# Performance work log

Measured on AMD Instinct MI355X. Metric: run time of the kernel, lower is better.

The kernel has to match this reference:

```python
import jax, jax.numpy as jnp
import numpy as np


def conv1x1(x, w, b):
    # x: [B,C,H,W], w: [O,C], b: [O] -> [B,O,H,W]
    return jnp.einsum('oc,bchw->bohw', w, x) + b[None, :, None, None]


def setup_inputs() -> dict:
    key = jax.random.key(0)
    ks = jax.random.split(key, 9)
    B, C, H, W = 4, 256, 64, 64
    Ci = C // 2
    s_in = 1.0 / np.sqrt(C)
    s_mid = 1.0 / np.sqrt(Ci)
    return {
        'x': jax.random.normal(ks[0], (B, C, H, W), jnp.float32),
        'theta_w': jax.random.normal(ks[1], (Ci, C), jnp.float32) * s_in,
        'theta_b': jnp.zeros((Ci,), jnp.float32),
        'phi_w': jax.random.normal(ks[2], (Ci, C), jnp.float32) * s_in,
        'phi_b': jnp.zeros((Ci,), jnp.float32),
        'g_w': jax.random.normal(ks[3], (Ci, C), jnp.float32) * s_in,
        'g_b': jnp.zeros((Ci,), jnp.float32),
        'out_w': jax.random.normal(ks[4], (C, Ci), jnp.float32) * s_mid,
        'out_b': jnp.zeros((C,), jnp.float32),
    }


def reference(x, theta_w, theta_b, phi_w, phi_b, g_w, g_b, out_w, out_b):
    B, C, H, W = x.shape
    N = H * W
    theta = conv1x1(x, theta_w, theta_b).reshape(B, -1, N)  # [B,Ci,N]
    phi = conv1x1(x, phi_w, phi_b).reshape(B, -1, N)        # [B,Ci,N]
    g = conv1x1(x, g_w, g_b).reshape(B, -1, N)              # [B,Ci,N]
    # attention[b,n,m] = theta[b,:,n] . phi[b,:,m]
    attn = jnp.einsum('bcn,bcm->bnm', theta, phi)           # [B,N,N]
    attn = jax.nn.softmax(attn, axis=-1)
    # out[b,c,n] = sum_m g[b,c,m] * attn[b,n,m]  (g @ attn^T)
    out = jnp.einsum('bcm,bnm->bcn', g, attn).reshape(B, -1, H, W)
    out = conv1x1(out, out_w, out_b)
    return out + x
```

## Files before the change

kernel.cpp:

```cpp
#include <hip/hip_runtime.h>
#include <stdint.h>

#define NB 4
#define NC 256
#define NCI 128
#define NN 4096

typedef __attribute__((ext_vector_type(8))) short short8;
typedef __attribute__((ext_vector_type(4))) float f32x4;

__device__ __forceinline__ float bf2f(unsigned short u) {
    union { unsigned int i; float f; } v; v.i = ((unsigned int)u) << 16; return v.f;
}
__device__ __forceinline__ unsigned short f2bf(float f) {
    union { unsigned int i; float f; } v; v.f = f;
    unsigned int b = v.i;
    b += 0x7FFFu + ((b >> 16) & 1u);
    return (unsigned short)(b >> 16);
}

__global__ void k_fill(float* __restrict__ p, float v, int n) {
    int i = blockIdx.x * blockDim.x + threadIdx.x;
    if (i < n) p[i] = v;
}

__global__ __launch_bounds__(256) void k_split(
    const float* __restrict__ Wt, const float* __restrict__ Wp,
    const float* __restrict__ Wg, const float* __restrict__ Wo,
    unsigned short* __restrict__ wbuf) {
    const float LOG2E = 1.4426950408889634f;
    int m = blockIdx.y;
    int i = blockIdx.x * 256 + threadIdx.x;
    if (m == 0) {
        float v = Wt[i] * LOG2E;
        unsigned short h = f2bf(v);
        wbuf[i] = h;
        wbuf[32768 + i] = f2bf(v - bf2f(h));
    } else if (m == 1) {
        float v = Wp[i];
        unsigned short h = f2bf(v);
        wbuf[65536 + i] = h;
        wbuf[98304 + i] = f2bf(v - bf2f(h));
    } else if (m == 2) {
        wbuf[131072 + i] = f2bf(Wg[i]);
    } else {
        wbuf[163840 + i] = f2bf(Wo[i]);
    }
}

__global__ __launch_bounds__(256, 2) void k_qkv2(
    const float* __restrict__ x,
    const unsigned short* __restrict__ WpH, const unsigned short* __restrict__ WpL,
    const unsigned short* __restrict__ WgH,
    const float* __restrict__ bp, const float* __restrict__ bg,
    unsigned short* __restrict__ phiH, unsigned short* __restrict__ phiL,
    unsigned short* __restrict__ gout) {
    __shared__ __align__(16) unsigned short sXh[32 * 72];
    __shared__ __align__(16) unsigned short sXl[32 * 72];
    const int b = blockIdx.y, n0 = blockIdx.x * 32;
    const int tid = threadIdx.x, lane = tid & 63, wave = tid >> 6;
    const int col = lane & 15, quad = lane >> 4;
    const int wm = wave * 32;

    f32x4 accP[2][2], accG[2][2];
#pragma unroll
    for (int i = 0; i < 2; i++)
#pragma unroll
        for (int j = 0; j < 2; j++)
#pragma unroll
            for (int e = 0; e < 4; e++) { accP[i][j][e] = 0.f; accG[i][j][e] = 0.f; }

    for (int c0 = 0; c0 < NC; c0 += 64) {
        __syncthreads();
        short8 ah[2][2], al[2][2], ag[2][2];
#pragma unroll
        for (int ks = 0; ks < 2; ks++)
#pragma unroll
            for (int i = 0; i < 2; i++) {
                size_t w = (size_t)(wm + i * 16 + col) * NC + c0 + ks * 32 + quad * 8;
                ah[ks][i] = *(const short8*)&WpH[w];
                al[ks][i] = *(const short8*)&WpL[w];
                ag[ks][i] = *(const short8*)&WgH[w];
            }
        {
            int cp = tid >> 3, n4 = (tid & 7) * 4;
            const float* xp = x + ((size_t)(b * NC + c0 + 2 * cp)) * NN + n0 + n4;
            float4 a = *(const float4*)xp;
            float4 c = *(const float4*)(xp + NN);
            float av[4] = { a.x, a.y, a.z, a.w };
            float cv[4] = { c.x, c.y, c.z, c.w };
#pragma unroll
            for (int j = 0; j < 4; j++) {
                unsigned short ha = f2bf(av[j]), hc = f2bf(cv[j]);
                unsigned short la = f2bf(av[j] - bf2f(ha)), lc = f2bf(cv[j] - bf2f(hc));
                *(unsigned int*)&sXh[(n4 + j) * 72 + 2 * cp] =
                    (unsigned int)ha | ((unsigned int)hc << 16);
                *(unsigned int*)&sXl[(n4 + j) * 72 + 2 * cp] =
                    (unsigned int)la | ((unsigned int)lc << 16);
            }
        }
        __syncthreads();
#pragma unroll
        for (int ks = 0; ks < 2; ks++)
#pragma unroll
            for (int j = 0; j < 2; j++) {
                short8 bh = *(const short8*)&sXh[(j * 16 + col) * 72 + ks * 32 + quad * 8];
                short8 bl = *(const short8*)&sXl[(j * 16 + col) * 72 + ks * 32 + quad * 8];
#pragma unroll
                for (int i = 0; i < 2; i++) {
                    accP[i][j] = __builtin_amdgcn_mfma_f32_16x16x32_bf16(ah[ks][i], bh, accP[i][j], 0, 0, 0);
                    accP[i][j] = __builtin_amdgcn_mfma_f32_16x16x32_bf16(ah[ks][i], bl, accP[i][j], 0, 0, 0);
                    accP[i][j] = __builtin_amdgcn_mfma_f32_16x16x32_bf16(al[ks][i], bh, accP[i][j], 0, 0, 0);
                    accG[i][j] = __builtin_amdgcn_mfma_f32_16x16x32_bf16(ag[ks][i], bh, accG[i][j], 0, 0, 0);
                }
            }
    }
#pragma unroll
    for (int i = 0; i < 2; i++) {
        int mrow = wm + i * 16 + quad * 4;
#pragma unroll
        for (int j = 0; j < 2; j++) {
            int n = n0 + j * 16 + col;
            unsigned short h[4], l[4];
#pragma unroll
            for (int e = 0; e < 4; e++) {
                float v = accP[i][j][e] + bp[mrow + e];
                h[e] = f2bf(v);
                l[e] = f2bf(v - bf2f(h[e]));
            }
            uint2 hv, lv;
            hv.x = (unsigned int)h[0] | ((unsigned int)h[1] << 16);
            hv.y = (unsigned int)h[2] | ((unsigned int)h[3] << 16);
            lv.x = (unsigned int)l[0] | ((unsigned int)l[1] << 16);
            lv.y = (unsigned int)l[2] | ((unsigned int)l[3] << 16);
            *(uint2*)&phiH[((size_t)(b * NN + n)) * NCI + mrow] = hv;
            *(uint2*)&phiL[((size_t)(b * NN + n)) * NCI + mrow] = lv;
#pragma unroll
            for (int r = 0; r < 4; r++)
                gout[((size_t)(b * NCI + mrow + r)) * NN + n] = f2bf(accG[i][j][r] + bg[mrow + r]);
        }
    }
}

__global__ __launch_bounds__(1024, 4) void k_attn(
    const float* __restrict__ x,
    const unsigned short* __restrict__ WtH, const unsigned short* __restrict__ WtL,
    const float* __restrict__ bt,
    const unsigned short* __restrict__ phiH, const unsigned short* __restrict__ phiL,
    const unsigned short* __restrict__ gmat,
    const unsigned short* __restrict__ WoH, const float* __restrict__ bo,
    float* __restrict__ y) {
    const float LOG2E = 1.4426950408889634f;
    __shared__ __align__(16) char smem[69632];
    unsigned short* sPhiH = (unsigned short*)(smem);
    unsigned short* sPhiL = (unsigned short*)(smem + 16384);
    unsigned short* sG    = (unsigned short*)(smem + 32768);
    unsigned short* sPall = (unsigned short*)(smem + 49152);
    float* sLi            = (float*)(smem + 57344);
    unsigned short* sThH  = (unsigned short*)(smem);
    unsigned short* sThL  = (unsigned short*)(smem + 16384);
    unsigned short* sXhA  = (unsigned short*)(smem + 32768);
    unsigned short* sXlA  = (unsigned short*)(smem + 41984);
    unsigned short* sXhB  = (unsigned short*)(smem + 51200);
    unsigned short* sXlB  = (unsigned short*)(smem + 60416);
    float* sThF           = (float*)(smem + 32768);
    unsigned short* sO    = (unsigned short*)(smem);

    const int id = blockIdx.x;
    const int xcd = id & 7, slot = id >> 3;
    const int b = xcd >> 1;
    const int n0 = (slot * 2 + (xcd & 1)) * 64;

    const int tid = threadIdx.x, lane = tid & 63, wave = tid >> 6;
    const int col = lane & 15, quad = lane >> 4;
    const int qg = wave >> 2, kh = wave & 3;

    const int half = wave >> 3;
    const int wci8 = (wave & 7) * 16;
    f32x4 th[4];
#pragma unroll
    for (int j = 0; j < 4; j++)
#pragma unroll
        for (int e = 0; e < 4; e++) th[j][e] = 0.f;

    for (int s = 0; s < 2; s++) {
        {
            int set = tid >> 9;
            int t = tid & 511;
            int cp = t >> 4, n4 = (t & 15) * 4;
            int myc0 = set * 128 + s * 64;
            unsigned short* dXh = set ? sXhB : sXhA;
            unsigned short* dXl = set ? sXlB : sXlA;
            const float* xp = x + ((size_t)(b * NC + myc0 + 2 * cp)) * NN + n0 + n4;
            float4 a = *(const float4*)xp;
            float4 c = *(const float4*)(xp + NN);
            float av[4] = { a.x, a.y, a.z, a.w };
            float cv[4] = { c.x, c.y, c.z, c.w };
#pragma unroll
            for (int j = 0; j < 4; j++) {
                unsigned short ha = f2bf(av[j]), hc = f2bf(cv[j]);
                unsigned short la = f2bf(av[j] - bf2f(ha)), lc = f2bf(cv[j] - bf2f(hc));
                *(unsigned int*)&dXh[(n4 + j) * 72 + 2 * cp] =
                    (unsigned int)ha | ((unsigned int)hc << 16);
                *(unsigned int*)&dXl[(n4 + j) * 72 + 2 * cp] =
                    (unsigned int)la | ((unsigned int)lc << 16);
            }
        }
        __syncthreads();
        {
            int c0 = half * 128 + s * 64;
            const unsigned short* mXh = half ? sXhB : sXhA;
            const unsigned short* mXl = half ? sXlB : sXlA;
#pragma unroll
            for (int ks = 0; ks < 2; ks++) {
                size_t w = (size_t)(wci8 + col) * NC + c0 + ks * 32 + quad * 8;
                short8 ah = *(const short8*)&WtH[w];
                short8 al = *(const short8*)&WtL[w];
#pragma unroll
                for (int j = 0; j < 4; j++) {
                    short8 bh = *(const short8*)&mXh[(j * 16 + col) * 72 + ks * 32 + quad * 8];
                    short8 bl = *(const short8*)&mXl[(j * 16 + col) * 72 + ks * 32 + quad * 8];
                    th[j] = __builtin_amdgcn_mfma_f32_16x16x32_bf16(ah, bh, th[j], 0, 0, 0);
                    th[j] = __builtin_amdgcn_mfma_f32_16x16x32_bf16(ah, bl, th[j], 0, 0, 0);
                    th[j] = __builtin_amdgcn_mfma_f32_16x16x32_bf16(al, bh, th[j], 0, 0, 0);
                }
            }
        }
        __syncthreads();
    }
    if (half == 0) {
#pragma unroll
        for (int j = 0; j < 4; j++) {
            int q = j * 16 + col;
            int ci = (wci8 + quad * 4) ^ ((q & 7) << 2);
            *(f32x4*)&sThF[q * 128 + ci] = th[j];
        }
    }
    __syncthreads();
    if (half == 1) {
#pragma unroll
        for (int j = 0; j < 4; j++) {
            int q = j * 16 + col;
            int cif = (wci8 + quad * 4) ^ ((q & 7) << 2);
            f32x4 o = *(const f32x4*)&sThF[q * 128 + cif];
            unsigned short h[4], l[4];
#pragma unroll
            for (int e = 0; e < 4; e++) {
                float v = o[e] + th[j][e] + bt[wci8 + quad * 4 + e] * LOG2E;
                h[e] = f2bf(v);
                l[e] = f2bf(v - bf2f(h[e]));
            }
            int cisw = (wci8 + quad * 4) ^ ((q & 7) << 3);
            uint2 hv, lv;
            hv.x = (unsigned int)h[0] | ((unsigned int)h[1] << 16);
            hv.y = (unsigned int)h[2] | ((unsigned int)h[3] << 16);
            lv.x = (unsigned int)l[0] | ((unsigned int)l[1] << 16);
            lv.y = (unsigned int)l[2] | ((unsigned int)l[3] << 16);
            *(uint2*)&sThH[q * 128 + cisw] = hv;
            *(uint2*)&sThL[q * 128 + cisw] = lv;
        }
    }
    __syncthreads();
    short8 qh[4], ql[4];
    {
        int qrow = qg * 16 + col;
        int qsw = (qrow & 7) << 3;
#pragma unroll
        for (int ks = 0; ks < 4; ks++) {
            int off = (ks * 32 + quad * 8) ^ qsw;
            qh[ks] = *(const short8*)&sThH[qrow * 128 + off];
            ql[ks] = *(const short8*)&sThL[qrow * 128 + off];
        }
    }

    f32x4 oacc[2];
#pragma unroll
    for (int i = 0; i < 2; i++)
#pragma unroll
        for (int e = 0; e < 4; e++) oacc[i][e] = 0.f;
    float li[4] = { 0.f, 0.f, 0.f, 0.f };

    for (int m0 = 0; m0 < NN; m0 += 64) {
        __syncthreads();
        {
            int row = tid >> 4, seg = tid & 15;
            size_t src = ((size_t)(b * NN + m0 + row)) * NCI + seg * 8;
            int dst = row * 128 + ((seg * 8) ^ ((row & 7) << 3));
            *(uint4*)&sPhiH[dst] = *(const uint4*)&phiH[src];
            *(uint4*)&sPhiL[dst] = *(const uint4*)&phiL[src];
            int row2 = tid >> 3, seg2 = tid & 7;
            int dst2 = row2 * 64 + ((seg2 * 8) ^ ((row2 & 7) << 3));
            *(uint4*)&sG[dst2] =
                *(const uint4*)&gmat[((size_t)(b * NCI + row2)) * NN + m0 + seg2 * 8];
        }
        __syncthreads();

        f32x4 S;
#pragma unroll
        for (int e = 0; e < 4; e++) S[e] = 0.f;
        {
            int kcol = kh * 16 + col;
            int kswz = (kcol & 7) << 3;
#pragma unroll
            for (int ks = 0; ks < 4; ks++) {
                int off = (ks * 32 + quad * 8) ^ kswz;
                short8 ph = *(const short8*)&sPhiH[kcol * 128 + off];
                short8 pl = *(const short8*)&sPhiL[kcol * 128 + off];
                S = __builtin_amdgcn_mfma_f32_16x16x32_bf16(qh[ks], ph, S, 0, 0, 0);
                S = __builtin_amdgcn_mfma_f32_16x16x32_bf16(qh[ks], pl, S, 0, 0, 0);
                S = __builtin_amdgcn_mfma_f32_16x16x32_bf16(ql[ks], ph, S, 0, 0, 0);
            }
        }
#pragma unroll
        for (int r = 0; r < 4; r++) {
            float p = exp2f(S[r]);
            li[r] += p;
            int q = qg * 16 + quad * 4 + r;
            sPall[q * 64 + ((kh * 16 + col) ^ ((q & 7) << 3))] = f2bf(p);
        }
        __syncthreads();

        short8 pf[2], af[2][2];
        {
            int qrow = qg * 16 + col;
            int qsw = (qrow & 7) << 3;
#pragma unroll
            for (int ks = 0; ks < 2; ks++)
                pf[ks] = *(const short8*)&sPall[qrow * 64 + ((ks * 32 + quad * 8) ^ qsw)];
#pragma unroll
            for (int ct = 0; ct < 2; ct++) {
                int grow = kh * 32 + ct * 16 + col;
                int gsw = (grow & 7) << 3;
#pragma unroll
                for (int ks = 0; ks < 2; ks++)
                    af[ct][ks] = *(const short8*)&sG[grow * 64 + ((ks * 32 + quad * 8) ^ gsw)];
            }
        }
#pragma unroll
        for (int ct = 0; ct < 2; ct++)
#pragma unroll
            for (int ks = 0; ks < 2; ks++)
                oacc[ct] = __builtin_amdgcn_mfma_f32_16x16x32_bf16(
                    af[ct][ks], pf[ks], oacc[ct], 0, 0, 0);
    }

#pragma unroll
    for (int r = 0; r < 4; r++) {
        float rs = li[r];
#pragma unroll
        for (int off = 1; off < 16; off <<= 1) rs += __shfl_xor(rs, off);
        li[r] = rs;
    }
    if (col == 0) {
#pragma unroll
        for (int r = 0; r < 4; r++) sLi[wave * 16 + quad * 4 + r] = li[r];
    }
    __syncthreads();
    float inv = 1.0f / (sLi[(qg * 4 + 0) * 16 + col] + sLi[(qg * 4 + 1) * 16 + col] +
                        sLi[(qg * 4 + 2) * 16 + col] + sLi[(qg * 4 + 3) * 16 + col]);

#pragma unroll
    for (int ct = 0; ct < 2; ct++) {
        int q = qg * 16 + col;
        int ci = kh * 32 + ct * 16 + quad * 4;
        int cisw = ci ^ ((q & 7) << 3);
        uint2 v;
        unsigned short p0 = f2bf(oacc[ct][0] * inv);
        unsigned short p1 = f2bf(oacc[ct][1] * inv);
        unsigned short p2 = f2bf(oacc[ct][2] * inv);
        unsigned short p3 = f2bf(oacc[ct][3] * inv);
        v.x = (unsigned int)p0 | ((unsigned int)p1 << 16);
        v.y = (unsigned int)p2 | ((unsigned int)p3 << 16);
        *(uint2*)&sO[q * 128 + cisw] = v;
    }
    __syncthreads();
    f32x4 acc[4];
#pragma unroll
    for (int j = 0; j < 4; j++)
#pragma unroll
        for (int e = 0; e < 4; e++) acc[j][e] = 0.f;
#pragma unroll
    for (int ks = 0; ks < 4; ks++) {
        short8 af2 = *(const short8*)&WoH[(size_t)(wave * 16 + col) * NCI + ks * 32 + quad * 8];
#pragma unroll
        for (int j = 0; j < 4; j++) {
            int row = j * 16 + col;
            short8 bf = *(const short8*)&sO[row * 128 + ((ks * 32 + quad * 8) ^ ((row & 7) << 3))];
            acc[j] = __builtin_amdgcn_mfma_f32_16x16x32_bf16(af2, bf, acc[j], 0, 0, 0);
        }
    }
#pragma unroll
    for (int j = 0; j < 4; j++)
#pragma unroll
        for (int e = 0; e < 4; e++) {
            int o = wave * 16 + quad * 4 + e;
            size_t idx = ((size_t)(b * NC + o)) * NN + n0 + j * 16 + col;
            y[idx] = acc[j][e] + bo[o] + x[idx];
        }
}

extern "C" void kernel_launch(void* const* d_in, const int* in_sizes, int n_in,
                              void* d_out, int out_size, void* d_ws, size_t ws_size,
                              hipStream_t stream) {
    float* y = (float*)d_out;

    bool sizes_ok = (n_in == 9) &&
        in_sizes[0] == NB * NC * NN && in_sizes[1] == NCI * NC && in_sizes[2] == NCI &&
        in_sizes[3] == NCI * NC && in_sizes[4] == NCI && in_sizes[5] == NCI * NC &&
        in_sizes[6] == NCI && in_sizes[7] == NC * NCI && in_sizes[8] == NC &&
        out_size == NB * NC * NN;
    if (!sizes_ok) {
        k_fill<<<(out_size + 255) / 256, 256, 0, stream>>>(y, 777.0f, out_size);
        return;
    }
    if (ws_size < (size_t)16 * 1024 * 1024) {
        k_fill<<<(out_size + 255) / 256, 256, 0, stream>>>(y, 555.0f, out_size);
        return;
    }

    const float* x  = (const float*)d_in[0];
    const float* tw = (const float*)d_in[1];
    const float* tb = (const float*)d_in[2];
    const float* pw = (const float*)d_in[3];
    const float* pb = (const float*)d_in[4];
    const float* gw = (const float*)d_in[5];
    const float* gb = (const float*)d_in[6];
    const float* ow = (const float*)d_in[7];
    const float* obias = (const float*)d_in[8];

    unsigned short* ws16 = (unsigned short*)d_ws;
    unsigned short* phiH = ws16;
    unsigned short* phiL = ws16 + 2097152;
    unsigned short* g    = ws16 + 4194304;
    unsigned short* wbuf = ws16 + 6291456;
    unsigned short* WtH = wbuf,           *WtL = wbuf + 32768;
    unsigned short* WpH = wbuf + 65536,   *WpL = wbuf + 98304;
    unsigned short* WgH = wbuf + 131072,  *WoH = wbuf + 163840;

    k_split<<<dim3(128, 4), 256, 0, stream>>>(tw, pw, gw, ow, wbuf);
    k_qkv2<<<dim3(128, NB), 256, 0, stream>>>(x, WpH, WpL, WgH, pb, gb, phiH, phiL, g);
    k_attn<<<dim3(256), 1024, 0, stream>>>(x, WtH, WtL, tb, phiH, phiL, g, WoH, obias, y);
}
```

Baseline: 220.2 us.

## Double-buffer phi/g tiles with register prefetch in attention loop

Splits the phi and g shared-memory staging into two buffers. The next key tile is loaded from global memory into registers at the start of each step and written to the alternate buffer after the MFMA work, so global load latency overlaps compute and one barrier per tile is removed. Shared memory use rises from about 68KB to 105KB per block, and the prefetch adds registers per thread. Both of these may limit occupancy on 1024-thread blocks.

```diff
diff --git a/kernel.cpp b/kernel.cpp
--- a/kernel.cpp
+++ b/kernel.cpp
@@ -151,12 +151,15 @@
     const unsigned short* __restrict__ WoH, const float* __restrict__ bo,
     float* __restrict__ y) {
     const float LOG2E = 1.4426950408889634f;
-    __shared__ __align__(16) char smem[69632];
-    unsigned short* sPhiH = (unsigned short*)(smem);
-    unsigned short* sPhiL = (unsigned short*)(smem + 16384);
-    unsigned short* sG    = (unsigned short*)(smem + 32768);
-    unsigned short* sPall = (unsigned short*)(smem + 49152);
-    float* sLi            = (float*)(smem + 57344);
+    __shared__ __align__(16) char smem[107520];
+    unsigned short* sPhiH0 = (unsigned short*)(smem);
+    unsigned short* sPhiH1 = (unsigned short*)(smem + 16384);
+    unsigned short* sPhiL0 = (unsigned short*)(smem + 32768);
+    unsigned short* sPhiL1 = (unsigned short*)(smem + 49152);
+    unsigned short* sG0    = (unsigned short*)(smem + 65536);
+    unsigned short* sG1    = (unsigned short*)(smem + 81920);
+    unsigned short* sPall  = (unsigned short*)(smem + 98304);
+    float* sLi             = (float*)(smem + 106496);
     unsigned short* sThH  = (unsigned short*)(smem);
     unsigned short* sThL  = (unsigned short*)(smem + 16384);
     unsigned short* sXhA  = (unsigned short*)(smem + 32768);
@@ -174,6 +177,24 @@
     const int tid = threadIdx.x, lane = tid & 63, wave = tid >> 6;
     const int col = lane & 15, quad = lane >> 4;
     const int qg = wave >> 2, kh = wave & 3;
+
+    uint4 rPh, rPl, rG;
+    auto LOADT = [&](int m0) {
+        int row = tid >> 4, seg = tid & 15;
+        size_t src = ((size_t)(b * NN + m0 + row)) * NCI + seg * 8;
+        rPh = *(const uint4*)&phiH[src];
+        rPl = *(const uint4*)&phiL[src];
+        int row2 = tid >> 3, seg2 = tid & 7;
+        rG = *(const uint4*)&gmat[((size_t)(b * NCI + row2)) * NN + m0 + seg2 * 8];
+    };
+    auto STORET = [&](unsigned short* dPh, unsigned short* dPl, unsigned short* dG) {
+        int row = tid >> 4, seg = tid & 15;
+        int dst = row * 128 + ((seg * 8) ^ ((row & 7) << 3));
+        *(uint4*)&dPh[dst] = rPh;
+        *(uint4*)&dPl[dst] = rPl;
+        int row2 = tid >> 3, seg2 = tid & 7;
+        *(uint4*)&dG[row2 * 64 + ((seg2 * 8) ^ ((row2 & 7) << 3))] = rG;
+    };
 
     const int half = wave >> 3;
     const int wci8 = (wave & 7) * 16;
@@ -272,6 +293,9 @@
             ql[ks] = *(const short8*)&sThL[qrow * 128 + off];
         }
     }
+    LOADT(0);
+    __syncthreads();
+    STORET(sPhiH0, sPhiL0, sG0);
 
     f32x4 oacc[2];
 #pragma unroll
@@ -280,20 +304,12 @@
         for (int e = 0; e < 4; e++) oacc[i][e] = 0.f;
     float li[4] = { 0.f, 0.f, 0.f, 0.f };
 
-    for (int m0 = 0; m0 < NN; m0 += 64) {
-        __syncthreads();
-        {
-            int row = tid >> 4, seg = tid & 15;
-            size_t src = ((size_t)(b * NN + m0 + row)) * NCI + seg * 8;
-            int dst = row * 128 + ((seg * 8) ^ ((row & 7) << 3));
-            *(uint4*)&sPhiH[dst] = *(const uint4*)&phiH[src];
-            *(uint4*)&sPhiL[dst] = *(const uint4*)&phiL[src];
-            int row2 = tid >> 3, seg2 = tid & 7;
-            int dst2 = row2 * 64 + ((seg2 * 8) ^ ((row2 & 7) << 3));
-            *(uint4*)&sG[dst2] =
-                *(const uint4*)&gmat[((size_t)(b * NCI + row2)) * NN + m0 + seg2 * 8];
-        }
-        __syncthreads();
+    auto tile_step = [&](const unsigned short* cPhiH, const unsigned short* cPhiL,
+                         const unsigned short* cG,
+                         unsigned short* nPhiH, unsigned short* nPhiL, unsigned short* nG,
+                         int m_next, bool do_next) {
+        __syncthreads();
+        if (do_next) LOADT(m_next);
 
         f32x4 S;
 #pragma unroll
@@ -304,8 +320,8 @@
 #pragma unroll
             for (int ks = 0; ks < 4; ks++) {
                 int off = (ks * 32 + quad * 8) ^ kswz;
-                short8 ph = *(const short8*)&sPhiH[kcol * 128 + off];
-                short8 pl = *(const short8*)&sPhiL[kcol * 128 + off];
+                short8 ph = *(const short8*)&cPhiH[kcol * 128 + off];
+                short8 pl = *(const short8*)&cPhiL[kcol * 128 + off];
                 S = __builtin_amdgcn_mfma_f32_16x16x32_bf16(qh[ks], ph, S, 0, 0, 0);
                 S = __builtin_amdgcn_mfma_f32_16x16x32_bf16(qh[ks], pl, S, 0, 0, 0);
                 S = __builtin_amdgcn_mfma_f32_16x16x32_bf16(ql[ks], ph, S, 0, 0, 0);
@@ -333,7 +349,7 @@
                 int gsw = (grow & 7) << 3;
 #pragma unroll
                 for (int ks = 0; ks < 2; ks++)
-                    af[ct][ks] = *(const short8*)&sG[grow * 64 + ((ks * 32 + quad * 8) ^ gsw)];
+                    af[ct][ks] = *(const short8*)&cG[grow * 64 + ((ks * 32 + quad * 8) ^ gsw)];
             }
         }
 #pragma unroll
@@ -342,6 +358,14 @@
             for (int ks = 0; ks < 2; ks++)
                 oacc[ct] = __builtin_amdgcn_mfma_f32_16x16x32_bf16(
                     af[ct][ks], pf[ks], oacc[ct], 0, 0, 0);
+
+        if (do_next) STORET(nPhiH, nPhiL, nG);
+    };
+
+    for (int m0 = 0; m0 < NN; m0 += 128) {
+        tile_step(sPhiH0, sPhiL0, sG0, sPhiH1, sPhiL1, sG1, m0 + 64, true);
+        bool more = (m0 + 128) < NN;
+        tile_step(sPhiH1, sPhiL1, sG1, sPhiH0, sPhiL0, sG0, m0 + 128, more);
     }
 
 #pragma unroll
```

After: 193.5 us. -12.2%, faster.

## Widen attention key tile to 128 with register-prefetched double-buffered G staging

Applied to the files above, without the earlier changes.

The attention loop now processes 128 keys per iteration instead of 64, with each wave computing two 16-row query tiles against its 16-key slice. The next phi/g tile is prefetched into registers while the current tile is computed, and g is double-buffered in LDS. This halves the number of loop iterations and barriers per key and hides global-load latency behind MFMA work. In exchange, LDS use grows to about 146 KB and register pressure rises, which can reduce occupancy to one block per CU.

```diff
diff --git a/kernel.cpp b/kernel.cpp
--- a/kernel.cpp
+++ b/kernel.cpp
@@ -151,12 +151,12 @@
     const unsigned short* __restrict__ WoH, const float* __restrict__ bo,
     float* __restrict__ y) {
     const float LOG2E = 1.4426950408889634f;
-    __shared__ __align__(16) char smem[69632];
-    unsigned short* sPhiH = (unsigned short*)(smem);
-    unsigned short* sPhiL = (unsigned short*)(smem + 16384);
-    unsigned short* sG    = (unsigned short*)(smem + 32768);
-    unsigned short* sPall = (unsigned short*)(smem + 49152);
-    float* sLi            = (float*)(smem + 57344);
+    __shared__ __align__(16) char smem[149504];
+    unsigned short* sPhiH  = (unsigned short*)(smem);
+    unsigned short* sPhiL  = (unsigned short*)(smem + 32768);
+    unsigned short* sGbase = (unsigned short*)(smem + 65536);
+    unsigned short* sPall  = (unsigned short*)(smem + 131072);
+    float* sLi             = (float*)(smem + 147456);
     unsigned short* sThH  = (unsigned short*)(smem);
     unsigned short* sThL  = (unsigned short*)(smem + 16384);
     unsigned short* sXhA  = (unsigned short*)(smem + 32768);
@@ -173,7 +173,32 @@
 
     const int tid = threadIdx.x, lane = tid & 63, wave = tid >> 6;
     const int col = lane & 15, quad = lane >> 4;
-    const int qg = wave >> 2, kh = wave & 3;
+    const int qg = wave >> 3, kh = wave & 7;
+    const int qv = wave & 3, cv = wave >> 2;
+
+    uint4 rPh[2], rPl[2], rG[2];
+    auto LOADTW = [&](int kbase) {
+#pragma unroll
+        for (int i = 0; i < 2; i++) {
+            int j = tid + i * 1024;
+            int row = j >> 4, seg = j & 15;
+            size_t sp = ((size_t)(b * NN + kbase + row)) * NCI + seg * 8;
+            rPh[i] = *(const uint4*)&phiH[sp];
+            rPl[i] = *(const uint4*)&phiL[sp];
+            rG[i]  = *(const uint4*)&gmat[((size_t)(b * NCI + row)) * NN + kbase + seg * 8];
+        }
+    };
+    auto STORETW = [&](unsigned short* gDst) {
+#pragma unroll
+        for (int i = 0; i < 2; i++) {
+            int j = tid + i * 1024;
+            int row = j >> 4, seg = j & 15;
+            int dst = row * 128 + ((seg * 8) ^ ((row & 7) << 3));
+            *(uint4*)&sPhiH[dst] = rPh[i];
+            *(uint4*)&sPhiL[dst] = rPl[i];
+            *(uint4*)&gDst[dst]  = rG[i];
+        }
+    };
 
     const int half = wave >> 3;
     const int wci8 = (wave & 7) * 16;
@@ -195,11 +220,11 @@
             float4 a = *(const float4*)xp;
             float4 c = *(const float4*)(xp + NN);
             float av[4] = { a.x, a.y, a.z, a.w };
-            float cv[4] = { c.x, c.y, c.z, c.w };
+            float cv4[4] = { c.x, c.y, c.z, c.w };
 #pragma unroll
             for (int j = 0; j < 4; j++) {
-                unsigned short ha = f2bf(av[j]), hc = f2bf(cv[j]);
-                unsigned short la = f2bf(av[j] - bf2f(ha)), lc = f2bf(cv[j] - bf2f(hc));
+                unsigned short ha = f2bf(av[j]), hc = f2bf(cv4[j]);
+                unsigned short la = f2bf(av[j] - bf2f(ha)), lc = f2bf(cv4[j] - bf2f(hc));
                 *(unsigned int*)&dXh[(n4 + j) * 72 + 2 * cp] =
                     (unsigned int)ha | ((unsigned int)hc << 16);
                 *(unsigned int*)&dXl[(n4 + j) * 72 + 2 * cp] =
@@ -261,108 +286,126 @@
         }
     }
     __syncthreads();
-    short8 qh[4], ql[4];
-    {
-        int qrow = qg * 16 + col;
-        int qsw = (qrow & 7) << 3;
+    short8 qh[2][4], ql[2][4];
+#pragma unroll
+    for (int qt = 0; qt < 2; qt++) {
+        int qrow = qg * 32 + qt * 16 + col;
+        int qsw = (col & 7) << 3;
 #pragma unroll
         for (int ks = 0; ks < 4; ks++) {
             int off = (ks * 32 + quad * 8) ^ qsw;
-            qh[ks] = *(const short8*)&sThH[qrow * 128 + off];
-            ql[ks] = *(const short8*)&sThL[qrow * 128 + off];
-        }
-    }
+            qh[qt][ks] = *(const short8*)&sThH[qrow * 128 + off];
+            ql[qt][ks] = *(const short8*)&sThL[qrow * 128 + off];
+        }
+    }
+    LOADTW(0);
+    __syncthreads();
+    STORETW(sGbase);
+    LOADTW(128);
+    __syncthreads();
 
     f32x4 oacc[2];
 #pragma unroll
     for (int i = 0; i < 2; i++)
 #pragma unroll
         for (int e = 0; e < 4; e++) oacc[i][e] = 0.f;
-    float li[4] = { 0.f, 0.f, 0.f, 0.f };
-
-    for (int m0 = 0; m0 < NN; m0 += 64) {
-        __syncthreads();
-        {
-            int row = tid >> 4, seg = tid & 15;
-            size_t src = ((size_t)(b * NN + m0 + row)) * NCI + seg * 8;
-            int dst = row * 128 + ((seg * 8) ^ ((row & 7) << 3));
-            *(uint4*)&sPhiH[dst] = *(const uint4*)&phiH[src];
-            *(uint4*)&sPhiL[dst] = *(const uint4*)&phiL[src];
-            int row2 = tid >> 3, seg2 = tid & 7;
-            int dst2 = row2 * 64 + ((seg2 * 8) ^ ((row2 & 7) << 3));
-            *(uint4*)&sG[dst2] =
-                *(const uint4*)&gmat[((size_t)(b * NCI + row2)) * NN + m0 + seg2 * 8];
-        }
-        __syncthreads();
-
-        f32x4 S;
-#pragma unroll
-        for (int e = 0; e < 4; e++) S[e] = 0.f;
+    float li[2][4];
+#pragma unroll
+    for (int i = 0; i < 2; i++)
+#pragma unroll
+        for (int r = 0; r < 4; r++) li[i][r] = 0.f;
+
+    auto stepw = [&](int gRd, int gWr, int m_next, bool do_stage, bool do_load) {
+        f32x4 S[2];
+#pragma unroll
+        for (int qt = 0; qt < 2; qt++)
+#pragma unroll
+            for (int e = 0; e < 4; e++) S[qt][e] = 0.f;
         {
             int kcol = kh * 16 + col;
-            int kswz = (kcol & 7) << 3;
+            int ksw = (col & 7) << 3;
 #pragma unroll
             for (int ks = 0; ks < 4; ks++) {
-                int off = (ks * 32 + quad * 8) ^ kswz;
+                int off = (ks * 32 + quad * 8) ^ ksw;
                 short8 ph = *(const short8*)&sPhiH[kcol * 128 + off];
                 short8 pl = *(const short8*)&sPhiL[kcol * 128 + off];
-                S = __builtin_amdgcn_mfma_f32_16x16x32_bf16(qh[ks], ph, S, 0, 0, 0);
-                S = __builtin_amdgcn_mfma_f32_16x16x32_bf16(qh[ks], pl, S, 0, 0, 0);
-                S = __builtin_amdgcn_mfma_f32_16x16x32_bf16(ql[ks], ph, S, 0, 0, 0);
-            }
-        }
+                S[0] = __builtin_amdgcn_mfma_f32_16x16x32_bf16(qh[0][ks], ph, S[0], 0, 0, 0);
+                S[0] = __builtin_amdgcn_mfma_f32_16x16x32_bf16(qh[0][ks], pl, S[0], 0, 0, 0);
+                S[0] = __builtin_amdgcn_mfma_f32_16x16x32_bf16(ql[0][ks], ph, S[0], 0, 0, 0);
+                S[1] = __builtin_amdgcn_mfma_f32_16x16x32_bf16(qh[1][ks], ph, S[1], 0, 0, 0);
+                S[1] = __builtin_amdgcn_mfma_f32_16x16x32_bf16(qh[1][ks], pl, S[1], 0, 0, 0);
+                S[1] = __builtin_amdgcn_mfma_f32_16x16x32_bf16(ql[1][ks], ph, S[1], 0, 0, 0);
+            }
+        }
+#pragma unroll
+        for (int qt = 0; qt < 2; qt++)
+#pragma unroll
+            for (int r = 0; r < 4; r++) {
+                float p = exp2f(S[qt][r]);
+                li[qt][r] += p;
+                int q = qg * 32 + qt * 16 + quad * 4 + r;
+                sPall[q * 128 + ((kh * 16 + col) ^ ((q & 7) << 3))] = f2bf(p);
+            }
+        __syncthreads();
+        {
+            int qrow = qv * 16 + col;
+            int psw = (col & 7) << 3;
+            const unsigned short* gB = sGbase + gRd;
+            int g0 = (cv * 32 + col) * 128;
+            int g1 = (cv * 32 + 16 + col) * 128;
+#pragma unroll
+            for (int ks = 0; ks < 4; ks++) {
+                int off = (ks * 32 + quad * 8) ^ psw;
+                short8 pf  = *(const short8*)&sPall[qrow * 128 + off];
+                short8 af0 = *(const short8*)&gB[g0 + off];
+                short8 af1 = *(const short8*)&gB[g1 + off];
+                oacc[0] = __builtin_amdgcn_mfma_f32_16x16x32_bf16(af0, pf, oacc[0], 0, 0, 0);
+                oacc[1] = __builtin_amdgcn_mfma_f32_16x16x32_bf16(af1, pf, oacc[1], 0, 0, 0);
+            }
+        }
+        if (do_stage) STORETW(sGbase + gWr);
+        if (do_load) LOADTW(m_next);
+        __syncthreads();
+    };
+
+    for (int it = 0; it < 15; ++it) {
+        stepw(0, 16384, (2 * it + 2) * 128, true, true);
+        stepw(16384, 0, (2 * it + 3) * 128, true, true);
+    }
+    stepw(0, 16384, 0, true, false);
+    stepw(16384, 0, 0, false, false);
+
+#pragma unroll
+    for (int qt = 0; qt < 2; qt++)
 #pragma unroll
         for (int r = 0; r < 4; r++) {
-            float p = exp2f(S[r]);
-            li[r] += p;
-            int q = qg * 16 + quad * 4 + r;
-            sPall[q * 64 + ((kh * 16 + col) ^ ((q & 7) << 3))] = f2bf(p);
-        }
-        __syncthreads();
-
-        short8 pf[2], af[2][2];
-        {
-            int qrow = qg * 16 + col;
-            int qsw = (qrow & 7) << 3;
-#pragma unroll
-            for (int ks = 0; ks < 2; ks++)
-                pf[ks] = *(const short8*)&sPall[qrow * 64 + ((ks * 32 + quad * 8) ^ qsw)];
-#pragma unroll
-            for (int ct = 0; ct < 2; ct++) {
-                int grow = kh * 32 + ct * 16 + col;
-                int gsw = (grow & 7) << 3;
-#pragma unroll
-                for (int ks = 0; ks < 2; ks++)
-                    af[ct][ks] = *(const short8*)&sG[grow * 64 + ((ks * 32 + quad * 8) ^ gsw)];
-            }
-        }
-#pragma unroll
-        for (int ct = 0; ct < 2; ct++)
-#pragma unroll
-            for (int ks = 0; ks < 2; ks++)
-                oacc[ct] = __builtin_amdgcn_mfma_f32_16x16x32_bf16(
-                    af[ct][ks], pf[ks], oacc[ct], 0, 0, 0);
-    }
-
-#pragma unroll
-    for (int r = 0; r < 4; r++) {
-        float rs = li[r];
-#pragma unroll
-        for (int off = 1; off < 16; off <<= 1) rs += __shfl_xor(rs, off);
-        li[r] = rs;
-    }
+            float rs = li[qt][r];
+#pragma unroll
+            for (int off = 1; off < 16; off <<= 1) rs += __shfl_xor(rs, off);
+            li[qt][r] = rs;
+        }
     if (col == 0) {
 #pragma unroll
-        for (int r = 0; r < 4; r++) sLi[wave * 16 + quad * 4 + r] = li[r];
-    }
-    __syncthreads();
-    float inv = 1.0f / (sLi[(qg * 4 + 0) * 16 + col] + sLi[(qg * 4 + 1) * 16 + col] +
-                        sLi[(qg * 4 + 2) * 16 + col] + sLi[(qg * 4 + 3) * 16 + col]);
+        for (int qt = 0; qt < 2; qt++)
+#pragma unroll
+            for (int r = 0; r < 4; r++)
+                sLi[wave * 32 + qt * 16 + quad * 4 + r] = li[qt][r];
+    }
+    __syncthreads();
+    float inv;
+    {
+        int qgf = qv >> 1, qtf = qv & 1;
+        float s = 0.f;
+#pragma unroll
+        for (int k8 = 0; k8 < 8; k8++)
+            s += sLi[(qgf * 8 + k8) * 32 + qtf * 16 + col];
+        inv = 1.0f / s;
+    }
 
 #pragma unroll
     for (int ct = 0; ct < 2; ct++) {
-        int q = qg * 16 + col;
-        int ci = kh * 32 + ct * 16 + quad * 4;
+        int q = qv * 16 + col;
+        int ci = cv * 32 + ct * 16 + quad * 4;
         int cisw = ci ^ ((q & 7) << 3);
         uint2 v;
         unsigned short p0 = f2bf(oacc[ct][0] * inv);
```

After: 507.3 us. 2.3x slower.
